# Kernel optimization log

Hardware: AMD Instinct MI355X
Metric: run time of the kernel (lower is better)

The kernel has to match this reference:

```python
import jax, jax.numpy as jnp
import numpy as np

VOCAB = 32000
EMB = 1024
BLOCK = 2048
B = 4


def setup_inputs() -> dict:
    key = jax.random.key(0)
    ks = jax.random.split(key, 10)
    s = EMB ** -0.5
    return {
        "idx": jax.random.randint(ks[0], (B, BLOCK), 0, VOCAB),
        "targets": jax.random.randint(ks[1], (B, BLOCK), 0, VOCAB),
        "tok_emb": jax.random.normal(ks[2], (VOCAB, EMB), jnp.float32),
        "pos_emb": jax.random.normal(ks[3], (BLOCK, EMB), jnp.float32),
        "Wk": jax.random.normal(ks[4], (EMB, EMB), jnp.float32) * s,
        "Wq": jax.random.normal(ks[5], (EMB, EMB), jnp.float32) * s,
        "Wv": jax.random.normal(ks[6], (EMB, EMB), jnp.float32) * s,
        "Wlm": jax.random.normal(ks[7], (EMB, VOCAB), jnp.float32) * s,
        "blm": jnp.zeros((VOCAB,), jnp.float32),
    }


def reference(idx, targets, tok_emb, pos_emb, Wk, Wq, Wv, Wlm, blm):
    B_, T = idx.shape
    x = tok_emb[idx] + pos_emb[:T]  # [B,T,C]
    C = x.shape[-1]
    k = x @ Wk  # [B,T,H]
    q = x @ Wq
    v = x @ Wv
    wei = jnp.einsum("bth,bsh->bts", q, k) * (C ** -0.5)  # [B,T,T]
    causal = jnp.tril(jnp.ones((T, T), bool))
    wei = jnp.where(causal, wei, -jnp.inf)
    wei = jax.nn.softmax(wei, axis=-1)
    out = jnp.einsum("bts,bsh->bth", wei, v)  # [B,T,H]
    logits = out @ Wlm + blm  # [B,T,V]
    logits2d = logits.reshape(B_ * T, -1)
    tgt = targets.reshape(B_ * T)
    logp = jax.nn.log_softmax(logits2d, axis=-1)
    loss = -jnp.mean(jnp.take_along_axis(logp, tgt[:, None], axis=1))
    return logits2d, loss
```

## Files before the change

kernel.cpp:

```cpp
#include <hip/hip_runtime.h>
#include <hip/hip_bf16.h>
#include <cstdint>

#define VOCAB 32000
#define EMB   1024
#define TLEN  2048
#define NB    4
#define MTOT  (NB*TLEN)

typedef __bf16 bf16;
typedef __bf16 bf16x8 __attribute__((ext_vector_type(8)));
typedef float  f32x4  __attribute__((ext_vector_type(4)));

__global__ void embed_kernel(const int* __restrict__ idx,
                             const float* __restrict__ tok,
                             const float* __restrict__ pos,
                             bf16* __restrict__ x)
{
    int gid = blockIdx.x * 256 + threadIdx.x;
    int r   = gid >> 7;
    int c0  = (gid & 127) << 3;
    int t   = r & (TLEN - 1);
    int tk  = idx[r];
    const float4* tp = reinterpret_cast<const float4*>(tok + (long)tk * EMB + c0);
    const float4* pp = reinterpret_cast<const float4*>(pos + (long)t  * EMB + c0);
    float4 a0 = tp[0], a1 = tp[1];
    float4 b0 = pp[0], b1 = pp[1];
    bf16x8 o;
    o[0] = (bf16)(a0.x + b0.x); o[1] = (bf16)(a0.y + b0.y);
    o[2] = (bf16)(a0.z + b0.z); o[3] = (bf16)(a0.w + b0.w);
    o[4] = (bf16)(a1.x + b1.x); o[5] = (bf16)(a1.y + b1.y);
    o[6] = (bf16)(a1.z + b1.z); o[7] = (bf16)(a1.w + b1.w);
    *reinterpret_cast<bf16x8*>(x + (long)r * EMB + c0) = o;
}

__global__ void transpose_conv_kernel(const float* __restrict__ W,
                                      bf16* __restrict__ Wt,
                                      int Kdim, int Ndim)
{
    __shared__ bf16 tile[64][65];
    int n0 = blockIdx.x * 64;
    int k0 = blockIdx.y * 64;
    int tid = threadIdx.x;
    int c  = tid & 63, r0 = tid >> 6;
#pragma unroll
    for (int i = 0; i < 16; ++i) {
        int r = r0 + i * 4;
        tile[r][c] = (bf16)W[(long)(k0 + r) * Ndim + n0 + c];
    }
    __syncthreads();
    int kc = tid & 63, nr0 = tid >> 6;
#pragma unroll
    for (int i = 0; i < 16; ++i) {
        int nr = nr0 + i * 4;
        Wt[(long)(n0 + nr) * Kdim + k0 + kc] = tile[kc][nr];
    }
}

__device__ __forceinline__ void gll16(const void* g, void* l)
{
    __builtin_amdgcn_global_load_lds(
        (const __attribute__((address_space(1))) unsigned int*)g,
        (__attribute__((address_space(3))) unsigned int*)l, 16, 0, 0);
}

__device__ __forceinline__ void stage256s(const bf16* __restrict__ gbase,
                                          int ld, int kt, bf16* lbase, int tid)
{
#pragma unroll
    for (int p = 0; p < 4; ++p) {
        int lin  = p * 512 + tid;
        int row  = lin >> 3;
        int slot = lin & 7;
        int ke   = ((slot ^ (row & 7)) << 3) + kt;
        gll16(gbase + (long)row * ld + ke, lbase + lin * 8);
    }
}

template<int CMODE>
__device__ __forceinline__ void gemm256_body(
    const bf16* __restrict__ A, int lda, long sA,
    const bf16* __restrict__ Bt, int ldb, long sB,
    bf16* __restrict__ C, int ldc, long sC, int K,
    int bx, int by, int zb, bf16* smem, int tid)
{
    bf16* As = smem;
    bf16* Bs = smem + 32768;

    const int lane = tid & 63, wid = tid >> 6;
    const int wr = wid >> 2, wc = wid & 3;
    const int l15 = lane & 15, hi = lane >> 4, l7 = lane & 7;

    const bf16* Ab = A  + (long)zb * sA + (long)(by * 256) * lda;
    const bf16* Bb = Bt + (long)zb * sB + (long)(bx * 256) * ldb;

    const int Keff = (CMODE == 2) ? ((by + 1) * 256) : K;
    const int NT   = Keff >> 6;

    f32x4 acc[8][4] = {};

    stage256s(Ab, lda, 0, As, tid);
    stage256s(Bb, ldb, 0, Bs, tid);
    __syncthreads();

#pragma unroll 1
    for (int t = 0; t < NT; ++t) {
        const int buf = t & 1;
        if (t + 1 < NT) {
            stage256s(Ab, lda, (t + 1) * 64, As + (buf ^ 1) * 16384, tid);
            stage256s(Bb, ldb, (t + 1) * 64, Bs + (buf ^ 1) * 16384, tid);
        }
        const bf16* Ap = As + buf * 16384 + (wr * 128) * 64;
        const bf16* Bp = Bs + buf * 16384 + (wc * 64) * 64;
#pragma unroll
        for (int ks = 0; ks < 2; ++ks) {
            const int ko = 8 * (((ks << 2) | hi) ^ l7);
            bf16x8 bfr[4];
#pragma unroll
            for (int n = 0; n < 4; ++n)
                bfr[n] = *(const bf16x8*)(Bp + (n * 16 + l15) * 64 + ko);
#pragma unroll
            for (int m = 0; m < 8; ++m) {
                bf16x8 af = *(const bf16x8*)(Ap + (m * 16 + l15) * 64 + ko);
#pragma unroll
                for (int n = 0; n < 4; ++n)
                    acc[m][n] = __builtin_amdgcn_mfma_f32_16x16x32_bf16(
                                    af, bfr[n], acc[m][n], 0, 0, 0);
            }
        }
        __syncthreads();
    }

    bf16* Cb = C + (long)zb * sC;
    const int colb = bx * 256 + wc * 64 + l15;
    const int rowb = by * 256 + wr * 128 + (hi << 2);
#pragma unroll
    for (int m = 0; m < 8; ++m)
#pragma unroll
        for (int n = 0; n < 4; ++n)
#pragma unroll
            for (int r = 0; r < 4; ++r)
                Cb[(long)(rowb + m * 16 + r) * ldc + colb + n * 16] =
                    (bf16)acc[m][n][r];
}

template<int CMODE>
__global__ __launch_bounds__(512)
void gemm256_bt(const bf16* __restrict__ A, int lda, long sA,
                const bf16* __restrict__ Bt, int ldb, long sB,
                bf16* __restrict__ C, int ldc, long sC, int K)
{
    extern __shared__ bf16 smem[];
    gemm256_body<CMODE>(A, lda, sA, Bt, ldb, sB, C, ldc, sC, K,
                        blockIdx.x, blockIdx.y, blockIdx.z, smem, threadIdx.x);
}

__global__ __launch_bounds__(512)
void fused_vt_s(const bf16* __restrict__ Wv_t, const bf16* __restrict__ x,
                bf16* __restrict__ v_t,
                const bf16* __restrict__ qk, bf16* __restrict__ S)
{
    extern __shared__ bf16 smem[];
    const int q = blockIdx.x, tid = threadIdx.x;
    if (q < 128) {
        gemm256_body<0>(Wv_t, EMB, 0, x, EMB, 0, v_t, MTOT, 0, EMB,
                        q & 31, q >> 5, 0, smem, tid);
    } else {
        int q2 = q - 128;
        int z = q2 / 36, t = q2 % 36;
        int by = 0, a = 0;
        while (a + by + 1 <= t) { a += by + 1; ++by; }
        int bx = t - a;
        gemm256_body<0>(qk, 2048, (long)TLEN * 2048,
                        qk + 1024, 2048, (long)TLEN * 2048,
                        S, TLEN, (long)TLEN * TLEN, EMB, bx, by, z, smem, tid);
    }
}

__global__ __launch_bounds__(512)
void fused_pv_wt(const bf16* __restrict__ P, const bf16* __restrict__ v_t,
                 bf16* __restrict__ att,
                 const float* __restrict__ Wlm, bf16* __restrict__ Wlm_t)
{
    extern __shared__ bf16 smem[];
    const int q = blockIdx.x, tid = threadIdx.x;
    if (q < 128) {
        gemm256_body<2>(P, TLEN, (long)TLEN * TLEN, v_t, MTOT, (long)TLEN,
                        att, EMB, (long)TLEN * EMB, TLEN,
                        q & 3, (q >> 2) & 7, q >> 5, smem, tid);
    } else {
        const int q2 = q - 128;
        const int n0 = (q2 % 125) * 256;
        const int k0 = (q2 / 125) * 64;
        bf16 (*tile)[257] = (bf16(*)[257])smem;
#pragma unroll
        for (int i = 0; i < 8; ++i) {
            int lin = i * 512 + tid;
            int r = lin >> 6, c4 = lin & 63;
            float4 v = *(const float4*)(Wlm + (long)(k0 + r) * VOCAB + n0 + c4 * 4);
            tile[r][c4 * 4 + 0] = (bf16)v.x;
            tile[r][c4 * 4 + 1] = (bf16)v.y;
            tile[r][c4 * 4 + 2] = (bf16)v.z;
            tile[r][c4 * 4 + 3] = (bf16)v.w;
        }
        __syncthreads();
#pragma unroll
        for (int i = 0; i < 4; ++i) {
            int lin = i * 512 + tid;
            int nr = lin >> 3, kc8 = (lin & 7) * 8;
            bf16x8 o;
#pragma unroll
            for (int j = 0; j < 8; ++j) o[j] = tile[kc8 + j][nr];
            *(bf16x8*)(Wlm_t + (long)(n0 + nr) * EMB + k0 + kc8) = o;
        }
    }
}

__global__ __launch_bounds__(512)
void gemm256_logits(const bf16* __restrict__ A, const bf16* __restrict__ Bt,
                    float* __restrict__ C, const float* __restrict__ bias,
                    float2* __restrict__ part)
{
    extern __shared__ bf16 smem[];
    bf16* As = smem;
    bf16* Bs = smem + 32768;

    const int tid  = threadIdx.x;
    const int lane = tid & 63, wid = tid >> 6;
    const int wr = wid >> 2, wc = wid & 3;
    const int l15 = lane & 15, hi = lane >> 4, l7 = lane & 7;

    const int wg = blockIdx.x;
    const int xcd = wg & 7, c = wg >> 3;
    const int nb = c >> 2;
    const int mb = xcd * 4 + (c & 3);

    const bf16* Ab = A  + (long)(mb * 256) * EMB;
    const bf16* Bb = Bt + (long)(nb * 256) * EMB;

    f32x4 acc[8][4] = {};

    stage256s(Ab, EMB, 0, As, tid);
    stage256s(Bb, EMB, 0, Bs, tid);
    __syncthreads();

    const int NT = EMB / 64;
#pragma unroll 1
    for (int t = 0; t < NT; ++t) {
        const int buf = t & 1;
        if (t + 1 < NT) {
            stage256s(Ab, EMB, (t + 1) * 64, As + (buf ^ 1) * 16384, tid);
            stage256s(Bb, EMB, (t + 1) * 64, Bs + (buf ^ 1) * 16384, tid);
        }
        const bf16* Ap = As + buf * 16384 + (wr * 128) * 64;
        const bf16* Bp = Bs + buf * 16384 + (wc * 64) * 64;
#pragma unroll
        for (int ks = 0; ks < 2; ++ks) {
            const int ko = 8 * (((ks << 2) | hi) ^ l7);
            bf16x8 bfr[4];
#pragma unroll
            for (int n = 0; n < 4; ++n)
                bfr[n] = *(const bf16x8*)(Bp + (n * 16 + l15) * 64 + ko);
#pragma unroll
            for (int m = 0; m < 8; ++m) {
                bf16x8 af = *(const bf16x8*)(Ap + (m * 16 + l15) * 64 + ko);
#pragma unroll
                for (int n = 0; n < 4; ++n)
                    acc[m][n] = __builtin_amdgcn_mfma_f32_16x16x32_bf16(
                                    af, bfr[n], acc[m][n], 0, 0, 0);
            }
        }
        __syncthreads();
    }

    float* pm = (float*)smem;
    float* ps = pm + 1024;

    const long colbase = (long)nb * 256 + wc * 64 + l15;
    float bv[4];
#pragma unroll
    for (int n = 0; n < 4; ++n) bv[n] = bias[colbase + n * 16];

    const long rowbase = (long)mb * 256 + wr * 128;
#pragma unroll
    for (int m = 0; m < 8; ++m) {
#pragma unroll
        for (int r = 0; r < 4; ++r) {
            float v0 = acc[m][0][r] + bv[0];
            float v1 = acc[m][1][r] + bv[1];
            float v2 = acc[m][2][r] + bv[2];
            float v3 = acc[m][3][r] + bv[3];
            long row = rowbase + m * 16 + (hi << 2) + r;
            float* Cp = C + row * (long)VOCAB + colbase;
            __builtin_nontemporal_store(v0, Cp);
            __builtin_nontemporal_store(v1, Cp + 16);
            __builtin_nontemporal_store(v2, Cp + 32);
            __builtin_nontemporal_store(v3, Cp + 48);

            float lm = fmaxf(fmaxf(v0, v1), fmaxf(v2, v3));
#pragma unroll
            for (int o = 1; o < 16; o <<= 1) lm = fmaxf(lm, __shfl_xor(lm, o));
            float sp = __expf(v0 - lm) + __expf(v1 - lm) +
                       __expf(v2 - lm) + __expf(v3 - lm);
#pragma unroll
            for (int o = 1; o < 16; o <<= 1) sp += __shfl_xor(sp, o);
            if (l15 == 0) {
                int rb = wr * 128 + m * 16 + (hi << 2) + r;
                pm[wc * 256 + rb] = lm;
                ps[wc * 256 + rb] = sp;
            }
        }
    }
    __syncthreads();
    if (tid < 256) {
        float m0 = pm[tid], m1 = pm[256 + tid], m2 = pm[512 + tid], m3 = pm[768 + tid];
        float M = fmaxf(fmaxf(m0, m1), fmaxf(m2, m3));
        float S = ps[tid] * __expf(m0 - M) + ps[256 + tid] * __expf(m1 - M) +
                  ps[512 + tid] * __expf(m2 - M) + ps[768 + tid] * __expf(m3 - M);
        part[((long)mb * 256 + tid) * 125 + nb] = make_float2(M, S);
    }
}

__global__ void softmax_causal_kernel(const bf16* __restrict__ S,
                                      bf16* __restrict__ P)
{
    const int r = blockIdx.x;
    const int t = r & (TLEN - 1);
    const int limit = ((t >> 8) + 1) << 8;
    const int tid = threadIdx.x;
    const int lane = tid & 63, wv = tid >> 6;
    const float scale = 0.03125f;
    const int c0 = tid * 8;

    float v[8];
    float m = -1e30f;
    if (c0 < limit) {
        bf16x8 sv = *(const bf16x8*)(S + (long)r * TLEN + c0);
#pragma unroll
        for (int i = 0; i < 8; ++i) {
            float x = (c0 + i <= t) ? (float)sv[i] * scale : -1e30f;
            v[i] = x;
            m = fmaxf(m, x);
        }
    } else {
#pragma unroll
        for (int i = 0; i < 8; ++i) v[i] = -1e30f;
    }
    __shared__ float red[4];
#pragma unroll
    for (int off = 32; off; off >>= 1) m = fmaxf(m, __shfl_xor(m, off));
    if (lane == 0) red[wv] = m;
    __syncthreads();
    m = fmaxf(fmaxf(red[0], red[1]), fmaxf(red[2], red[3]));
    __syncthreads();

    float s = 0.f;
#pragma unroll
    for (int i = 0; i < 8; ++i) { v[i] = __expf(v[i] - m); s += v[i]; }
#pragma unroll
    for (int off = 32; off; off >>= 1) s += __shfl_xor(s, off);
    if (lane == 0) red[wv] = s;
    __syncthreads();
    s = red[0] + red[1] + red[2] + red[3];
    float inv = 1.0f / s;
    if (c0 < limit) {
        bf16x8 o;
#pragma unroll
        for (int i = 0; i < 8; ++i) o[i] = (bf16)(v[i] * inv);
        *(bf16x8*)(P + (long)r * TLEN + c0) = o;
    }
}

__global__ void loss_combine_kernel(const float2* __restrict__ part,
                                    const float* __restrict__ logits,
                                    const int* __restrict__ tgt,
                                    float* __restrict__ bsum)
{
    const int tid = threadIdx.x;
    const int row = blockIdx.x * 256 + tid;
    const int lane = tid & 63, wv = tid >> 6;
    const float2* p = part + (long)row * 125;
    float M = -1e30f, S = 0.f;
    for (int i = 0; i < 125; ++i) {
        float2 v = p[i];
        if (v.x <= M) S += v.y * __expf(v.x - M);
        else { S = S * __expf(M - v.x) + v.y; M = v.x; }
    }
    float lse = M + __logf(S);
    float l = lse - logits[(long)row * VOCAB + tgt[row]];
#pragma unroll
    for (int off = 32; off; off >>= 1) l += __shfl_xor(l, off);
    __shared__ float red[4];
    if (lane == 0) red[wv] = l;
    __syncthreads();
    if (tid == 0) bsum[blockIdx.x] = red[0] + red[1] + red[2] + red[3];
}

__global__ void loss_final_kernel(const float* __restrict__ bsum,
                                  float* __restrict__ out)
{
    const int lane = threadIdx.x;
    float s = (lane < 32) ? bsum[lane] : 0.f;
#pragma unroll
    for (int off = 32; off; off >>= 1) s += __shfl_xor(s, off);
    if (lane == 0) out[0] = s * (1.0f / MTOT);
}

extern "C" void kernel_launch(void* const* d_in, const int* in_sizes, int n_in,
                              void* d_out, int out_size, void* d_ws, size_t ws_size,
                              hipStream_t stream)
{
    const int*   idx = (const int*)  d_in[0];
    const int*   tgt = (const int*)  d_in[1];
    const float* tok = (const float*)d_in[2];
    const float* pos = (const float*)d_in[3];
    const float* Wk  = (const float*)d_in[4];
    const float* Wq  = (const float*)d_in[5];
    const float* Wv  = (const float*)d_in[6];
    const float* Wlm = (const float*)d_in[7];
    const float* blm = (const float*)d_in[8];
    float* out = (float*)d_out;

    char* ws = (char*)d_ws;
    if (ws_size < (size_t)140 * 1024 * 1024) return;

    bf16*   x     = (bf16*)(ws);
    bf16*   qk    = (bf16*)(ws + (16l << 20));
    bf16*   v_t   = (bf16*)(ws + (48l << 20));
    bf16*   S     = (bf16*)(ws + (64l << 20));
    bf16*   Wqk_t = (bf16*)(ws + (96l << 20));
    bf16*   Wv_t  = (bf16*)(ws + (100l << 20));
    bf16*   att   = (bf16*)(ws);
    bf16*   P     = (bf16*)(ws + (16l << 20));
    bf16*   Wlm_t = (bf16*)(ws + (64l << 20));
    float2* part  = (float2*)(ws + (127l << 20));
    float*  bsum  = (float*)(ws + (135l << 20));

    embed_kernel<<<dim3(MTOT * EMB / 8 / 256), 256, 0, stream>>>(idx, tok, pos, x);

    transpose_conv_kernel<<<dim3(16, 16), 256, 0, stream>>>(Wq, Wqk_t, EMB, EMB);
    transpose_conv_kernel<<<dim3(16, 16), 256, 0, stream>>>(Wk, Wqk_t + 1024 * 1024, EMB, EMB);
    transpose_conv_kernel<<<dim3(16, 16), 256, 0, stream>>>(Wv, Wv_t, EMB, EMB);

    gemm256_bt<0><<<dim3(2048 / 256, MTOT / 256, 1), 512, 131072, stream>>>(
        x, EMB, 0, Wqk_t, EMB, 0, qk, 2048, 0, EMB);

    fused_vt_s<<<dim3(272), 512, 131072, stream>>>(Wv_t, x, v_t, qk, S);

    softmax_causal_kernel<<<dim3(MTOT), 256, 0, stream>>>(S, P);

    fused_pv_wt<<<dim3(2128), 512, 131072, stream>>>(P, v_t, att, Wlm, Wlm_t);

    gemm256_logits<<<dim3(4000), 512, 131072, stream>>>(att, Wlm_t, out, blm, part);

    loss_combine_kernel<<<dim3(32), 256, 0, stream>>>(part, out, tgt, bsum);
    loss_final_kernel<<<dim3(1), 64, 0, stream>>>(bsum, out + (long)MTOT * VOCAB);
}
```

Baseline: 834.1 us.

## Make logits GEMM loop over four M tiles per workgroup with cross-tile prefetch

The logits GEMM now launches 1000 workgroups, and each one iterates over four consecutive 256-row M tiles for a fixed N block. The next tile's first K slice is prefetched during the last K step of the current tile. The softmax partial reduction now gets its own LDS region, which raises LDS from 128 KiB to 136 KiB, and the nontemporal stores move after the reduction. The goal is to hide per-tile prologue and epilogue latency and reuse B-tile locality, at the cost of fewer workgroups and less parallelism across the 256 CUs.

```diff
diff --git a/kernel.cpp b/kernel.cpp
--- a/kernel.cpp
+++ b/kernel.cpp
@@ -224,100 +224,112 @@
     extern __shared__ bf16 smem[];
     bf16* As = smem;
     bf16* Bs = smem + 32768;
+    float* pm = (float*)(smem + 65536);
+    float* ps = pm + 1024;
 
     const int tid  = threadIdx.x;
     const int lane = tid & 63, wid = tid >> 6;
     const int wr = wid >> 2, wc = wid & 3;
     const int l15 = lane & 15, hi = lane >> 4, l7 = lane & 7;
 
-    const int wg = blockIdx.x;
-    const int xcd = wg & 7, c = wg >> 3;
-    const int nb = c >> 2;
-    const int mb = xcd * 4 + (c & 3);
-
-    const bf16* Ab = A  + (long)(mb * 256) * EMB;
+    const int wg  = blockIdx.x;
+    const int xcd = wg & 7;
+    const int nb  = wg >> 3;
+
     const bf16* Bb = Bt + (long)(nb * 256) * EMB;
-
-    f32x4 acc[8][4] = {};
-
-    stage256s(Ab, EMB, 0, As, tid);
-    stage256s(Bb, EMB, 0, Bs, tid);
-    __syncthreads();
-
-    const int NT = EMB / 64;
-#pragma unroll 1
-    for (int t = 0; t < NT; ++t) {
-        const int buf = t & 1;
-        if (t + 1 < NT) {
-            stage256s(Ab, EMB, (t + 1) * 64, As + (buf ^ 1) * 16384, tid);
-            stage256s(Bb, EMB, (t + 1) * 64, Bs + (buf ^ 1) * 16384, tid);
-        }
-        const bf16* Ap = As + buf * 16384 + (wr * 128) * 64;
-        const bf16* Bp = Bs + buf * 16384 + (wc * 64) * 64;
-#pragma unroll
-        for (int ks = 0; ks < 2; ++ks) {
-            const int ko = 8 * (((ks << 2) | hi) ^ l7);
-            bf16x8 bfr[4];
-#pragma unroll
-            for (int n = 0; n < 4; ++n)
-                bfr[n] = *(const bf16x8*)(Bp + (n * 16 + l15) * 64 + ko);
-#pragma unroll
-            for (int m = 0; m < 8; ++m) {
-                bf16x8 af = *(const bf16x8*)(Ap + (m * 16 + l15) * 64 + ko);
-#pragma unroll
-                for (int n = 0; n < 4; ++n)
-                    acc[m][n] = __builtin_amdgcn_mfma_f32_16x16x32_bf16(
-                                    af, bfr[n], acc[m][n], 0, 0, 0);
-            }
-        }
-        __syncthreads();
-    }
-
-    float* pm = (float*)smem;
-    float* ps = pm + 1024;
 
     const long colbase = (long)nb * 256 + wc * 64 + l15;
     float bv[4];
 #pragma unroll
     for (int n = 0; n < 4; ++n) bv[n] = bias[colbase + n * 16];
 
-    const long rowbase = (long)mb * 256 + wr * 128;
-#pragma unroll
-    for (int m = 0; m < 8; ++m) {
-#pragma unroll
-        for (int r = 0; r < 4; ++r) {
-            float v0 = acc[m][0][r] + bv[0];
-            float v1 = acc[m][1][r] + bv[1];
-            float v2 = acc[m][2][r] + bv[2];
-            float v3 = acc[m][3][r] + bv[3];
-            long row = rowbase + m * 16 + (hi << 2) + r;
-            float* Cp = C + row * (long)VOCAB + colbase;
-            __builtin_nontemporal_store(v0, Cp);
-            __builtin_nontemporal_store(v1, Cp + 16);
-            __builtin_nontemporal_store(v2, Cp + 32);
-            __builtin_nontemporal_store(v3, Cp + 48);
-
-            float lm = fmaxf(fmaxf(v0, v1), fmaxf(v2, v3));
-#pragma unroll
-            for (int o = 1; o < 16; o <<= 1) lm = fmaxf(lm, __shfl_xor(lm, o));
-            float sp = __expf(v0 - lm) + __expf(v1 - lm) +
-                       __expf(v2 - lm) + __expf(v3 - lm);
-#pragma unroll
-            for (int o = 1; o < 16; o <<= 1) sp += __shfl_xor(sp, o);
-            if (l15 == 0) {
-                int rb = wr * 128 + m * 16 + (hi << 2) + r;
-                pm[wc * 256 + rb] = lm;
-                ps[wc * 256 + rb] = sp;
+    stage256s(A + (long)(xcd * 4) * 256 * EMB, EMB, 0, As, tid);
+    stage256s(Bb, EMB, 0, Bs, tid);
+    __syncthreads();
+
+#pragma unroll 1
+    for (int tile = 0; tile < 4; ++tile) {
+        const int mb = xcd * 4 + tile;
+        const bf16* Ab  = A + (long)mb * 256 * EMB;
+        const bf16* AbN = A + (long)(mb + 1) * 256 * EMB;
+
+        f32x4 acc[8][4] = {};
+
+#pragma unroll 1
+        for (int t = 0; t < 16; ++t) {
+            const int buf = t & 1;
+            if (t < 15) {
+                stage256s(Ab, EMB, (t + 1) * 64, As + (buf ^ 1) * 16384, tid);
+                stage256s(Bb, EMB, (t + 1) * 64, Bs + (buf ^ 1) * 16384, tid);
+            } else if (tile < 3) {
+                stage256s(AbN, EMB, 0, As + (buf ^ 1) * 16384, tid);
+                stage256s(Bb,  EMB, 0, Bs + (buf ^ 1) * 16384, tid);
             }
-        }
-    }
-    __syncthreads();
-    if (tid < 256) {
-        float m0 = pm[tid], m1 = pm[256 + tid], m2 = pm[512 + tid], m3 = pm[768 + tid];
-        float M = fmaxf(fmaxf(m0, m1), fmaxf(m2, m3));
-        float S = ps[tid] * __expf(m0 - M) + ps[256 + tid] * __expf(m1 - M) +
-                  ps[512 + tid] * __expf(m2 - M) + ps[768 + tid] * __expf(m3 - M);
-        part[((long)mb * 256 + tid) * 125 + nb] = make_float2(M, S);
+            const bf16* Ap = As + buf * 16384 + (wr * 128) * 64;
+            const bf16* Bp = Bs + buf * 16384 + (wc * 64) * 64;
+#pragma unroll
+            for (int ks = 0; ks < 2; ++ks) {
+                const int ko = 8 * (((ks << 2) | hi) ^ l7);
+                bf16x8 bfr[4];
+#pragma unroll
+                for (int n = 0; n < 4; ++n)
+                    bfr[n] = *(const bf16x8*)(Bp + (n * 16 + l15) * 64 + ko);
+#pragma unroll
+                for (int m = 0; m < 8; ++m) {
+                    bf16x8 af = *(const bf16x8*)(Ap + (m * 16 + l15) * 64 + ko);
+#pragma unroll
+                    for (int n = 0; n < 4; ++n)
+                        acc[m][n] = __builtin_amdgcn_mfma_f32_16x16x32_bf16(
+                                        af, bfr[n], acc[m][n], 0, 0, 0);
+                }
+            }
+            __syncthreads();
+        }
+
+        const long rowbase = (long)mb * 256 + wr * 128;
+#pragma unroll
+        for (int m = 0; m < 8; ++m) {
+#pragma unroll
+            for (int r = 0; r < 4; ++r) {
+                float v0 = acc[m][0][r] + bv[0];
+                float v1 = acc[m][1][r] + bv[1];
+                float v2 = acc[m][2][r] + bv[2];
+                float v3 = acc[m][3][r] + bv[3];
+                float lm = fmaxf(fmaxf(v0, v1), fmaxf(v2, v3));
+#pragma unroll
+                for (int o = 1; o < 16; o <<= 1) lm = fmaxf(lm, __shfl_xor(lm, o));
+                float sp = __expf(v0 - lm) + __expf(v1 - lm) +
+                           __expf(v2 - lm) + __expf(v3 - lm);
+#pragma unroll
+                for (int o = 1; o < 16; o <<= 1) sp += __shfl_xor(sp, o);
+                if (l15 == 0) {
+                    int rb = wr * 128 + m * 16 + (hi << 2) + r;
+                    pm[wc * 256 + rb] = lm;
+                    ps[wc * 256 + rb] = sp;
+                }
+            }
+        }
+        __syncthreads();
+        if (tid < 256) {
+            float m0 = pm[tid], m1 = pm[256 + tid];
+            float m2 = pm[512 + tid], m3 = pm[768 + tid];
+            float M = fmaxf(fmaxf(m0, m1), fmaxf(m2, m3));
+            float Sv = ps[tid] * __expf(m0 - M) + ps[256 + tid] * __expf(m1 - M) +
+                       ps[512 + tid] * __expf(m2 - M) + ps[768 + tid] * __expf(m3 - M);
+            part[((long)mb * 256 + tid) * 125 + nb] = make_float2(M, Sv);
+        }
+#pragma unroll
+        for (int m = 0; m < 8; ++m) {
+#pragma unroll
+            for (int r = 0; r < 4; ++r) {
+                long row = rowbase + m * 16 + (hi << 2) + r;
+                float* Cp = C + row * (long)VOCAB + colbase;
+                __builtin_nontemporal_store(acc[m][0][r] + bv[0], Cp);
+                __builtin_nontemporal_store(acc[m][1][r] + bv[1], Cp + 16);
+                __builtin_nontemporal_store(acc[m][2][r] + bv[2], Cp + 32);
+                __builtin_nontemporal_store(acc[m][3][r] + bv[3], Cp + 48);
+            }
+        }
     }
 }
 
@@ -451,7 +463,7 @@
 
     fused_pv_wt<<<dim3(2128), 512, 131072, stream>>>(P, v_t, att, Wlm, Wlm_t);
 
-    gemm256_logits<<<dim3(4000), 512, 131072, stream>>>(att, Wlm_t, out, blm, part);
+    gemm256_logits<<<dim3(1000), 512, 139264, stream>>>(att, Wlm_t, out, blm, part);
 
     loss_combine_kernel<<<dim3(32), 256, 0, stream>>>(part, out, tgt, bsum);
     loss_final_kernel<<<dim3(1), 64, 0, stream>>>(bsum, out + (long)MTOT * VOCAB);
```

Result: slower. 1.087 ms (+30.3%).
